# Kernel optimization log

Measured on AMD Instinct MI355X. Metric: run time of the kernel, lower is better.

The kernel has to match this reference:

```python
import jax, jax.numpy as jnp
import numpy as np

DIM = 1024          # dim_feature
NUM_CLUSTERS = 8
N_PER = 4096        # patches per cluster (equal-size clusters)
NUM_SAMPLE = 1024   # num_sample_feature
QDIM = 128          # q projection dim
# sample_ratio = NUM_SAMPLE / (NUM_CLUSTERS*N_PER) = 1/32 -> top_k per cluster
TOPK = int(np.rint(N_PER * NUM_SAMPLE / (NUM_CLUSTERS * N_PER)))  # 128


def setup_inputs() -> dict:
    key = jax.random.key(0)
    ks = jax.random.split(key, 6)
    s = 1.0 / np.sqrt(DIM)
    return {
        "cluster_features": jax.random.normal(ks[0], (NUM_CLUSTERS, N_PER, DIM), jnp.float32),
        "key_feats": jax.random.normal(ks[1], (NUM_CLUSTERS, 1, DIM), jnp.float32),
        "q_w": jax.random.normal(ks[2], (QDIM, DIM), jnp.float32) * s,
        "q_b": jax.random.normal(ks[3], (QDIM,), jnp.float32) * 0.01,
        "v_w": jax.random.normal(ks[4], (DIM, DIM), jnp.float32) * s,
        "v_b": jax.random.normal(ks[5], (DIM,), jnp.float32) * 0.01,
    }


def reference(cluster_features, key_feats, q_w, q_b, v_w, v_b):
    scale_q = jnp.sqrt(jnp.float32(QDIM))

    def per_cluster(feats, key_feat):
        # NonLocalRanking with top_k=TOPK, top_fuse=False (adaptive path)
        Q = feats @ q_w.T + q_b            # [N, 128]
        qk = key_feat @ q_w.T + q_b        # [1, 128]
        A = (Q @ qk.T) / scale_q           # [N, 1]
        A = jax.nn.softmax(A, axis=0)      # softmax over patches (dim 0)
        _, idx = jax.lax.top_k(A[:, 0], TOPK)
        top_feats = feats[idx]             # [TOPK, DIM]
        V = feats @ v_w.T + v_b            # [N, DIM]
        fusion = (A.T @ V)[0]              # [DIM]
        return top_feats, fusion

    tops, fus = jax.vmap(per_cluster)(cluster_features, key_feats)
    selected = tops.reshape(-1, DIM)       # [NUM_CLUSTERS*TOPK, DIM] == [NUM_SAMPLE, DIM]
    # module pads/truncates to NUM_SAMPLE; here it is exactly NUM_SAMPLE
    selected = selected[:NUM_SAMPLE]
    return selected, fus
```

## Files before the change

kernel.cpp:

```cpp
#include <hip/hip_runtime.h>
#include <math.h>


#define DIM   1024
#define NC    8
#define NPER  4096
#define QD    128
#define TOPK  128
#define K1B   128

typedef unsigned long long u64;
typedef __attribute__((ext_vector_type(2))) unsigned long long ull2;

__global__ __launch_bounds__(256) void k0_prep(
    const float* __restrict__ key_feats, const float* __restrict__ q_w,
    const float* __restrict__ q_b, float* __restrict__ w_all)
{
    const int c  = blockIdx.x >> 2, jc = blockIdx.x & 3;
    const int tid = threadIdx.x;
    __shared__ float part[256];
    __shared__ float qs[QD];

    {
        const int k = tid >> 1, half = tid & 1;
        const float4* qr4 = (const float4*)(q_w + (size_t)k * DIM + half * 512);
        const float4* kf4 = (const float4*)(key_feats + (size_t)c * DIM + half * 512);
        float s = 0.f;
        #pragma unroll 16
        for (int j = 0; j < 128; ++j) {
            float4 a = qr4[j], b = kf4[j];
            s += a.x*b.x + a.y*b.y + a.z*b.z + a.w*b.w;
        }
        part[tid] = s;
    }
    __syncthreads();
    if (tid < QD) qs[tid] = part[2*tid] + part[2*tid+1] + q_b[tid];
    __syncthreads();

    const int j = jc * 256 + tid;
    float s = 0.f;
    #pragma unroll 16
    for (int k = 0; k < QD; ++k)
        s += q_w[(size_t)k * DIM + j] * qs[k];
    w_all[c * DIM + j] = s * 0.08838834764831845f;
}

__global__ __launch_bounds__(256, 4) void k1_main(
    const float* __restrict__ feats, const float* __restrict__ w_all,
    u64* __restrict__ keys,
    float* __restrict__ pacc,
    float* __restrict__ pm, float* __restrict__ pz)
{
    const int c    = blockIdx.y;
    const int blk  = blockIdx.x;
    const int tid  = threadIdx.x;
    const int lane = tid & 63;
    const int wave = tid >> 6;

    const float4* w4 = (const float4*)(w_all + c * DIM);
    float4 wv[4];
    #pragma unroll
    for (int q = 0; q < 4; ++q) wv[q] = w4[lane + 64*q];

    float4 acc[4];
    #pragma unroll
    for (int q = 0; q < 4; ++q) acc[q] = make_float4(0.f, 0.f, 0.f, 0.f);
    float m = -INFINITY, Z = 0.f;

    const int wslot = blk * 4 + wave;
    const float* fc = feats + (size_t)c * NPER * DIM;

    float4 fA[4], fB[4];
    {
        const float4* f4 = (const float4*)(fc + (size_t)wslot * DIM);
        #pragma unroll
        for (int q = 0; q < 4; ++q) fA[q] = f4[lane + 64*q];
    }

    #define K1_PROCESS(FREG, ROW)                                              \
    do {                                                                       \
        float p = 0.f;                                                         \
        _Pragma("unroll")                                                      \
        for (int q = 0; q < 4; ++q)                                            \
            p += FREG[q].x*wv[q].x + FREG[q].y*wv[q].y +                       \
                 FREG[q].z*wv[q].z + FREG[q].w*wv[q].w;                        \
        _Pragma("unroll")                                                      \
        for (int off = 32; off > 0; off >>= 1) p += __shfl_xor(p, off, 64);    \
        if (lane == 0) {                                                       \
            unsigned int b = __float_as_uint(p);                               \
            unsigned int u = b ^ ((b & 0x80000000u) ? 0xFFFFFFFFu : 0x80000000u); \
            keys[c * NPER + (ROW)] = ((u64)u << 32) | (unsigned int)(~(ROW));  \
        }                                                                      \
        const float mn   = fmaxf(m, p);                                        \
        const float sOld = __expf(m - mn);                                     \
        const float t    = __expf(p - mn);                                     \
        Z = Z * sOld + t;                                                      \
        _Pragma("unroll")                                                      \
        for (int q = 0; q < 4; ++q) {                                          \
            acc[q].x = acc[q].x * sOld + t * FREG[q].x;                        \
            acc[q].y = acc[q].y * sOld + t * FREG[q].y;                        \
            acc[q].z = acc[q].z * sOld + t * FREG[q].z;                        \
            acc[q].w = acc[q].w * sOld + t * FREG[q].w;                        \
        }                                                                      \
        m = mn;                                                                \
    } while (0)

    for (int it = 0; it < 8; it += 2) {
        const int r0 = wslot + 512 * it;
        {
            const float4* f4 = (const float4*)(fc + (size_t)(r0 + 512) * DIM);
            #pragma unroll
            for (int q = 0; q < 4; ++q) fB[q] = f4[lane + 64*q];
        }
        K1_PROCESS(fA, r0);
        if (it + 2 < 8) {
            const float4* f4 = (const float4*)(fc + (size_t)(r0 + 1024) * DIM);
            #pragma unroll
            for (int q = 0; q < 4; ++q) fA[q] = f4[lane + 64*q];
        }
        K1_PROCESS(fB, r0 + 512);
    }
    #undef K1_PROCESS

    __shared__ float sm[4], sz[4];
    __shared__ float sacc[4][DIM];
    if (lane == 0) { sm[wave] = m; sz[wave] = Z; }
    #pragma unroll
    for (int q = 0; q < 4; ++q)
        ((float4*)sacc[wave])[lane + 64*q] = acc[q];
    __syncthreads();

    const float mb = fmaxf(fmaxf(sm[0], sm[1]), fmaxf(sm[2], sm[3]));
    const float e0 = __expf(sm[0] - mb), e1 = __expf(sm[1] - mb);
    const float e2 = __expf(sm[2] - mb), e3 = __expf(sm[3] - mb);
    float4 a0 = ((float4*)sacc[0])[tid];
    float4 a1 = ((float4*)sacc[1])[tid];
    float4 a2 = ((float4*)sacc[2])[tid];
    float4 a3 = ((float4*)sacc[3])[tid];
    float4 o;
    o.x = a0.x*e0 + a1.x*e1 + a2.x*e2 + a3.x*e3;
    o.y = a0.y*e0 + a1.y*e1 + a2.y*e2 + a3.y*e3;
    o.z = a0.z*e0 + a1.z*e1 + a2.z*e2 + a3.z*e3;
    o.w = a0.w*e0 + a1.w*e1 + a2.w*e2 + a3.w*e3;
    ((float4*)(pacc + (size_t)(c * K1B + blk) * DIM))[tid] = o;
    if (tid == 0) {
        pm[c * K1B + blk] = mb;
        pz[c * K1B + blk] = sz[0]*e0 + sz[1]*e1 + sz[2]*e2 + sz[3]*e3;
    }
}

__global__ __launch_bounds__(256) void k2_combine(
    const float* __restrict__ pacc, const float* __restrict__ pm,
    const float* __restrict__ pz, float* __restrict__ g)
{
    const int c = blockIdx.y, jb = blockIdx.x;
    const int tid  = threadIdx.x;
    const int slot = tid & 63;
    const int bg   = tid >> 6;
    __shared__ float spm[K1B], spz[K1B], swe[K1B];
    __shared__ float szc;
    __shared__ float4 sred[3][64];

    if (tid < K1B) spm[tid] = pm[c*K1B + tid];
    else spz[tid - K1B] = pz[c*K1B + tid - K1B];
    __syncthreads();
    float mc = -INFINITY;
    for (int b = 0; b < K1B; ++b) mc = fmaxf(mc, spm[b]);
    if (tid < K1B) swe[tid] = __expf(spm[tid] - mc);
    __syncthreads();
    if (tid == 0) {
        float z = 0.f;
        for (int b = 0; b < K1B; ++b) z += spz[b] * swe[b];
        szc = z;
    }

    const int jbase = jb * 256 + slot * 4;
    float4 a = make_float4(0.f, 0.f, 0.f, 0.f);
    #pragma unroll
    for (int k = 0; k < 32; ++k) {
        const int b = bg * 32 + k;
        const float e = swe[b];
        float4 v = *(const float4*)(pacc + (size_t)(c*K1B + b) * DIM + jbase);
        a.x += e*v.x; a.y += e*v.y; a.z += e*v.z; a.w += e*v.w;
    }
    if (bg) sred[bg-1][slot] = a;
    __syncthreads();
    if (bg == 0) {
        float4 t0 = sred[0][slot], t1 = sred[1][slot], t2 = sred[2][slot];
        const float inv = 1.0f / szc;
        float4 o;
        o.x = (a.x + t0.x + t1.x + t2.x) * inv;
        o.y = (a.y + t0.y + t1.y + t2.y) * inv;
        o.z = (a.z + t0.z + t1.z + t2.z) * inv;
        o.w = (a.w + t0.w + t1.w + t2.w) * inv;
        *(float4*)(g + c * DIM + jbase) = o;
    }
}

__global__ __launch_bounds__(256) void k3a_rank(
    const u64* __restrict__ keys, int* __restrict__ part)
{
    const int iblk = blockIdx.x, js = blockIdx.y, c = blockIdx.z;
    const int tid = threadIdx.x;
    __shared__ u64 lk[512];
    ((float4*)lk)[tid] = ((const float4*)(keys + c * NPER + js * 512))[tid];

    const int ibase = iblk * 1024;
    u64 ki[4];
    #pragma unroll
    for (int q = 0; q < 4; ++q) ki[q] = keys[c * NPER + ibase + tid + 256*q];
    __syncthreads();

    int cnt0 = 0, cnt1 = 0, cnt2 = 0, cnt3 = 0;
    const ull2* lk2 = (const ull2*)lk;
    #pragma unroll 4
    for (int jt = 0; jt < 256; ++jt) {
        ull2 kj = lk2[jt];
        cnt0 += (kj.x > ki[0]) + (kj.y > ki[0]);
        cnt1 += (kj.x > ki[1]) + (kj.y > ki[1]);
        cnt2 += (kj.x > ki[2]) + (kj.y > ki[2]);
        cnt3 += (kj.x > ki[3]) + (kj.y > ki[3]);
    }
    int* dst = part + ((js * NC + c) << 12) + ibase + tid;
    dst[0]   = cnt0; dst[256] = cnt1; dst[512] = cnt2; dst[768] = cnt3;
}

__global__ __launch_bounds__(256) void k3b_scatter(
    const int* __restrict__ part, int* __restrict__ sel)
{
    const int c = blockIdx.y;
    const int i = blockIdx.x * 256 + threadIdx.x;
    int r = 0;
    #pragma unroll
    for (int js = 0; js < 8; ++js) r += part[((js * NC + c) << 12) + i];
    if (r < TOPK) sel[c * TOPK + r] = i;
}

__global__ __launch_bounds__(256) void k4_gather(
    const float* __restrict__ feats, const int* __restrict__ sel,
    float* __restrict__ out_sel)
{
    const int b = blockIdx.x;
    const int c = b >> 7;
    const int i = sel[b];
    const float4* src = (const float4*)(feats + ((size_t)c * NPER + i) * DIM);
    float4* dst = (float4*)(out_sel + (size_t)b * DIM);
    dst[threadIdx.x] = src[threadIdx.x];
}

__global__ __launch_bounds__(256) void k5_fusion(
    const float* __restrict__ v_w, const float* __restrict__ v_b,
    const float* __restrict__ g, float* __restrict__ fus)
{
    __shared__ float4 sg[NC][256];
    const int tid = threadIdx.x, lane = tid & 63, wave = tid >> 6;
    for (int t = tid; t < NC * 256; t += 256)
        ((float4*)sg)[t] = ((const float4*)g)[t];
    __syncthreads();

    const int row0 = blockIdx.x * 8 + wave * 2;
    for (int rr = 0; rr < 2; ++rr) {
        const int o = row0 + rr;
        const float4* vr = (const float4*)(v_w + (size_t)o * DIM);
        float4 v[4];
        #pragma unroll
        for (int u = 0; u < 4; ++u) v[u] = vr[lane + 64*u];
        float p[NC];
        #pragma unroll
        for (int cc = 0; cc < NC; ++cc) {
            float s = 0.f;
            #pragma unroll
            for (int u = 0; u < 4; ++u) {
                float4 gv = sg[cc][lane + 64*u];
                s += v[u].x*gv.x + v[u].y*gv.y + v[u].z*gv.z + v[u].w*gv.w;
            }
            p[cc] = s;
        }
        #pragma unroll
        for (int off = 32; off > 0; off >>= 1) {
            #pragma unroll
            for (int cc = 0; cc < NC; ++cc) p[cc] += __shfl_xor(p[cc], off, 64);
        }
        if (lane == 0) {
            const float b = v_b[o];
            #pragma unroll
            for (int cc = 0; cc < NC; ++cc) fus[cc * DIM + o] = p[cc] + b;
        }
    }
}

extern "C" void kernel_launch(void* const* d_in, const int* in_sizes, int n_in,
                              void* d_out, int out_size, void* d_ws, size_t ws_size,
                              hipStream_t stream) {
    const float* feats     = (const float*)d_in[0];
    const float* key_feats = (const float*)d_in[1];
    const float* q_w       = (const float*)d_in[2];
    const float* q_b       = (const float*)d_in[3];
    const float* v_w       = (const float*)d_in[4];
    const float* v_b       = (const float*)d_in[5];
    float* out      = (float*)d_out;
    float* out_sel  = out;
    float* out_fus  = out + (size_t)1024 * 1024;

    u64*   keys   = (u64*)d_ws;
    float* pacc   = (float*)(keys + NC * NPER);
    float* pm     = pacc + (size_t)NC * K1B * DIM;
    float* pz     = pm + NC * K1B;
    float* g      = pz + NC * K1B;
    float* w_all  = g + NC * DIM;
    int*   part   = (int*)(w_all + NC * DIM);
    int*   sel    = part + 8 * NC * NPER;

    k0_prep    <<<dim3(NC * 4),    256, 0, stream>>>(key_feats, q_w, q_b, w_all);
    k1_main    <<<dim3(K1B, NC),   256, 0, stream>>>(feats, w_all, keys, pacc, pm, pz);
    k2_combine <<<dim3(4, NC),     256, 0, stream>>>(pacc, pm, pz, g);
    k3a_rank   <<<dim3(4, 8, NC),  256, 0, stream>>>(keys, part);
    k3b_scatter<<<dim3(16, NC),    256, 0, stream>>>(part, sel);
    k4_gather  <<<dim3(NC * TOPK), 256, 0, stream>>>(feats, sel, out_sel);
    k5_fusion  <<<dim3(128),       256, 0, stream>>>(v_w, v_b, g, out_fus);
}
```

Baseline: 275.1 us.

## Branch online softmax on new max and fuse rank scatter with row gather

The online-softmax update in the main streaming kernel now branches on whether the new score exceeds the running max, so each row needs only one exp and the common case skips rescaling the accumulator. The scatter and gather kernels are merged: each block collects its selected rows in shared memory and copies them straight to the output, which removes one launch and the intermediate index buffer. The cost is that the merged kernel has only 128 blocks, each copying a variable number of rows in sequence, so the gather runs with less parallelism and uneven load.

```diff
diff --git a/kernel.cpp b/kernel.cpp
--- a/kernel.cpp
+++ b/kernel.cpp
@@ -91,18 +91,28 @@
             unsigned int u = b ^ ((b & 0x80000000u) ? 0xFFFFFFFFu : 0x80000000u); \
             keys[c * NPER + (ROW)] = ((u64)u << 32) | (unsigned int)(~(ROW));  \
         }                                                                      \
-        const float mn   = fmaxf(m, p);                                        \
-        const float sOld = __expf(m - mn);                                     \
-        const float t    = __expf(p - mn);                                     \
-        Z = Z * sOld + t;                                                      \
-        _Pragma("unroll")                                                      \
-        for (int q = 0; q < 4; ++q) {                                          \
-            acc[q].x = acc[q].x * sOld + t * FREG[q].x;                        \
-            acc[q].y = acc[q].y * sOld + t * FREG[q].y;                        \
-            acc[q].z = acc[q].z * sOld + t * FREG[q].z;                        \
-            acc[q].w = acc[q].w * sOld + t * FREG[q].w;                        \
+        if (p > m) {                  \
+            const float sOld = __expf(m - p);                                  \
+            Z = Z * sOld + 1.f;                                                \
+            _Pragma("unroll")                                                  \
+            for (int q = 0; q < 4; ++q) {                                      \
+                acc[q].x = acc[q].x * sOld + FREG[q].x;                        \
+                acc[q].y = acc[q].y * sOld + FREG[q].y;                        \
+                acc[q].z = acc[q].z * sOld + FREG[q].z;                        \
+                acc[q].w = acc[q].w * sOld + FREG[q].w;                        \
+            }                                                                  \
+            m = p;                                                             \
+        } else {                                                               \
+            const float t = __expf(p - m);                                     \
+            Z += t;                                                            \
+            _Pragma("unroll")                                                  \
+            for (int q = 0; q < 4; ++q) {                                      \
+                acc[q].x += t * FREG[q].x;                                     \
+                acc[q].y += t * FREG[q].y;                                     \
+                acc[q].z += t * FREG[q].z;                                     \
+                acc[q].w += t * FREG[q].w;                                     \
+            }                                                                  \
         }                                                                      \
-        m = mn;                                                                \
     } while (0)
 
     for (int it = 0; it < 8; it += 2) {
@@ -225,27 +235,33 @@
     dst[0]   = cnt0; dst[256] = cnt1; dst[512] = cnt2; dst[768] = cnt3;
 }
 
-__global__ __launch_bounds__(256) void k3b_scatter(
-    const int* __restrict__ part, int* __restrict__ sel)
+__global__ __launch_bounds__(256) void k3b_gather(
+    const int* __restrict__ part, const float* __restrict__ feats,
+    float* __restrict__ out_sel)
 {
     const int c = blockIdx.y;
     const int i = blockIdx.x * 256 + threadIdx.x;
+    const int tid = threadIdx.x;
+    __shared__ int list_i[TOPK], list_r[TOPK];
+    __shared__ int cnt;
+    if (tid == 0) cnt = 0;
+    __syncthreads();
+
     int r = 0;
     #pragma unroll
     for (int js = 0; js < 8; ++js) r += part[((js * NC + c) << 12) + i];
-    if (r < TOPK) sel[c * TOPK + r] = i;
-}
-
-__global__ __launch_bounds__(256) void k4_gather(
-    const float* __restrict__ feats, const int* __restrict__ sel,
-    float* __restrict__ out_sel)
-{
-    const int b = blockIdx.x;
-    const int c = b >> 7;
-    const int i = sel[b];
-    const float4* src = (const float4*)(feats + ((size_t)c * NPER + i) * DIM);
-    float4* dst = (float4*)(out_sel + (size_t)b * DIM);
-    dst[threadIdx.x] = src[threadIdx.x];
+    if (r < TOPK) {
+        const int s = atomicAdd(&cnt, 1);
+        list_i[s] = i; list_r[s] = r;
+    }
+    __syncthreads();
+
+    const int n = cnt;
+    for (int s = 0; s < n; ++s) {
+        const float4* src = (const float4*)(feats + ((size_t)c * NPER + list_i[s]) * DIM);
+        float4* dst = (float4*)(out_sel + ((size_t)c * TOPK + list_r[s]) * DIM);
+        dst[tid] = src[tid];
+    }
 }
 
 __global__ __launch_bounds__(256) void k5_fusion(
@@ -309,13 +325,11 @@
     float* g      = pz + NC * K1B;
     float* w_all  = g + NC * DIM;
     int*   part   = (int*)(w_all + NC * DIM);
-    int*   sel    = part + 8 * NC * NPER;
 
     k0_prep    <<<dim3(NC * 4),    256, 0, stream>>>(key_feats, q_w, q_b, w_all);
     k1_main    <<<dim3(K1B, NC),   256, 0, stream>>>(feats, w_all, keys, pacc, pm, pz);
     k2_combine <<<dim3(4, NC),     256, 0, stream>>>(pacc, pm, pz, g);
     k3a_rank   <<<dim3(4, 8, NC),  256, 0, stream>>>(keys, part);
-    k3b_scatter<<<dim3(16, NC),    256, 0, stream>>>(part, sel);
-    k4_gather  <<<dim3(NC * TOPK), 256, 0, stream>>>(feats, sel, out_sel);
+    k3b_gather <<<dim3(16, NC),    256, 0, stream>>>(part, feats, out_sel);
     k5_fusion  <<<dim3(128),       256, 0, stream>>>(v_w, v_b, g, out_fus);
 }
```

New measurement: 257.3 us. 6.5% less time.
